# Performance work log

Hardware: AMD Instinct MI355X
Metric: run time of the kernel (lower is better)

## Reference

```python
import jax, jax.numpy as jnp
import numpy as np

NUM_HEADS = 8
HEAD_DIM = 16
HIDDEN = 128  # NUM_HEADS * HEAD_DIM
EPS = 1e-12
NEG_BIG = -1000000.0


def setup_inputs() -> dict:
    key = jax.random.key(0)
    ks = jax.random.split(key, 12)
    bz, n, na, hid = 16, 1024, 32, HIDDEN
    std = 0.02
    return {
        "h": jax.random.normal(ks[0], (bz, n, hid), dtype=jnp.float32),
        "message": jax.random.normal(ks[1], (bz, n, na, hid), dtype=jnp.float32),
        "mask": jax.random.randint(ks[2], (bz, n, na, 1), 0, 2).astype(jnp.float32),
        "qW": jax.random.normal(ks[3], (hid, hid), dtype=jnp.float32) * std,
        "qb": jnp.zeros((hid,), jnp.float32),
        "kW": jax.random.normal(ks[4], (hid, hid), dtype=jnp.float32) * std,
        "kb": jnp.zeros((hid,), jnp.float32),
        "vW": jax.random.normal(ks[5], (hid, hid), dtype=jnp.float32) * std,
        "vb": jnp.zeros((hid,), jnp.float32),
        "dW": jax.random.normal(ks[6], (hid, hid), dtype=jnp.float32) * std,
        "db": jnp.zeros((hid,), jnp.float32),
        "ln_w": jnp.ones((hid,), jnp.float32),
        "ln_b": jnp.zeros((hid,), jnp.float32),
    }


def _layernorm(x, w, b):
    u = jnp.mean(x, axis=-1, keepdims=True)
    s = jnp.mean((x - u) ** 2, axis=-1, keepdims=True)
    return w * ((x - u) / jnp.sqrt(s + EPS)) + b


def reference(h, message, mask, qW, qb, kW, kb, vW, vb, dW, db, ln_w, ln_b):
    bz, n, na, hid = message.shape
    # projections (torch Linear math: x @ W^T + b; here weights stored as [in,out])
    q = h @ qW + qb                              # [b,n,hid]
    k = message @ kW + kb                        # [b,n,na,hid]
    v = jax.nn.relu(message @ vW + vb)           # [b,n,na,hid]
    # split heads
    qh = q.reshape(bz, n, NUM_HEADS, HEAD_DIM)                 # [b,n,h,d] (q_len=1)
    kh = k.reshape(bz, n, na, NUM_HEADS, HEAD_DIM)             # [b,n,k,h,d]
    vh = v.reshape(bz, n, na, NUM_HEADS, HEAD_DIM)
    m = mask[..., 0][:, :, None, :]                            # [b,n,1,k] broadcast over heads
    scores = jnp.einsum("bnhd,bnkhd->bnhk", qh, kh)
    scores = scores / jnp.sqrt(jnp.asarray(HEAD_DIM, scores.dtype)) * m
    scores = jnp.where(scores == 0.0, NEG_BIG, scores)
    probs = jax.nn.softmax(scores, axis=-1) * m                # [b,n,h,k]
    ctx = jnp.einsum("bnhk,bnkhd->bnhd", probs, vh).reshape(bz, n, hid)
    hidden_states = ctx @ dW + db
    return _layernorm(hidden_states + h, ln_w, ln_b)
```

## Files before the change

kernel.cpp:

```cpp
#include <hip/hip_runtime.h>

typedef short  short4v  __attribute__((ext_vector_type(4)));
typedef float  float4v  __attribute__((ext_vector_type(4)));

#define NA   32
#define HID  128
#define NH   8
#define TPB  8
#define KSTR 132

__device__ __forceinline__ unsigned short f2bf(float f) {
  unsigned int u = __float_as_uint(f);
  return (unsigned short)((u + 0x7FFFu + ((u >> 16) & 1u)) >> 16);
}

__global__ __launch_bounds__(256, 2) void soft_attn_mfma(
    const float* __restrict__ h, const float* __restrict__ msg,
    const float* __restrict__ mask,
    const float* __restrict__ qW, const float* __restrict__ qb,
    const float* __restrict__ kW, const float* __restrict__ kb,
    const float* __restrict__ vW, const float* __restrict__ vb,
    const float* __restrict__ dW, const float* __restrict__ db,
    const float* __restrict__ lnw, const float* __restrict__ lnb,
    float* __restrict__ out, int n_tokens)
{
  const int t    = threadIdx.x;
  const int lane = t & 63;
  const int w    = t >> 6;
  const int n0   = w * 32;
  const int lm   = lane & 15;
  const int lg   = lane >> 4;
  const int tok0 = blockIdx.x * TPB;
  if (tok0 >= n_tokens) return;

  __shared__ __align__(16) short s_msgF[16 * 64 * 4];
  __shared__ __align__(16) short s_hF  [ 8 * 64 * 4];
  __shared__ __align__(16) short s_ctxF[ 8 * 64 * 4];
  __shared__ __align__(16) float s_qall[TPB * HID];
  __shared__ __align__(16) float s_hall[TPB * HID];
  __shared__ __align__(16) float s_dall[TPB * HID];
  __shared__ __align__(16) float s_k[NA * KSTR];
  __shared__ __align__(16) float s_v[NA * KSTR];
  __shared__ __align__(16) float s_p[NH * NA];

  {
    ((float4v*)s_hall)[t] = ((const float4v*)(h + (size_t)tok0 * HID))[t];
#pragma unroll
    for (int j = 0; j < 2; ++j) {
      const int s  = t + 256 * j;
      const int f  = s >> 6;
      const int sl = s & 63;
      const int m  = sl & 15, kg = sl >> 4;
      short4v sv = {0, 0, 0, 0};
      if (m < TPB) {
        const float4v hv = *(const float4v*)(h + (size_t)(tok0 + m) * HID + f * 16 + kg * 4);
#pragma unroll
        for (int e = 0; e < 4; ++e) sv[e] = (short)f2bf(hv[e]);
      } else {
        ((short4v*)s_ctxF)[s] = sv;
      }
      ((short4v*)s_hF)[s] = sv;
    }
  }

  {
    short4v Bq[2][8];
    float qb2[2];
#pragma unroll
    for (int nt = 0; nt < 2; ++nt) {
      qb2[nt] = qb[n0 + nt * 16 + lm];
#pragma unroll
      for (int ks = 0; ks < 8; ++ks) {
        short4v bv;
#pragma unroll
        for (int e = 0; e < 4; ++e)
          bv[e] = (short)f2bf(qW[(size_t)(ks * 16 + lg * 4 + e) * HID + n0 + nt * 16 + lm]);
        Bq[nt][ks] = bv;
      }
    }
    __syncthreads();
    float4v accq[2];
#pragma unroll
    for (int nt = 0; nt < 2; ++nt) accq[nt] = (float4v){qb2[nt], qb2[nt], qb2[nt], qb2[nt]};
#pragma unroll
    for (int ks = 0; ks < 8; ++ks) {
      const short4v aq = ((const short4v*)s_hF)[ks * 64 + lane];
#pragma unroll
      for (int nt = 0; nt < 2; ++nt)
        accq[nt] = __builtin_amdgcn_mfma_f32_16x16x16bf16_1k(aq, Bq[nt][ks], accq[nt], 0, 0, 0);
    }
#pragma unroll
    for (int nt = 0; nt < 2; ++nt)
#pragma unroll
      for (int r = 0; r < 4; ++r) {
        const int row = lg * 4 + r;
        if (row < TPB) s_qall[row * HID + n0 + nt * 16 + lm] = accq[nt][r];
      }
  }

  short4v Bk[2][8], Bv[2][8];
  float kb2[2], vb2[2];
#pragma unroll
  for (int nt = 0; nt < 2; ++nt) {
    kb2[nt] = kb[n0 + nt * 16 + lm];
    vb2[nt] = vb[n0 + nt * 16 + lm];
#pragma unroll
    for (int ks = 0; ks < 8; ++ks) {
      short4v bk, bv;
#pragma unroll
      for (int e = 0; e < 4; ++e) {
        const size_t widx = (size_t)(ks * 16 + lg * 4 + e) * HID + n0 + nt * 16 + lm;
        bk[e] = (short)f2bf(kW[widx]);
        bv[e] = (short)f2bf(vW[widx]);
      }
      Bk[nt][ks] = bk; Bv[nt][ks] = bv;
    }
  }

  float4v P[4];
#pragma unroll
  for (int j = 0; j < 4; ++j) {
    const int f = w + 4 * j, mt = f >> 3, ks = f & 7;
    P[j] = *(const float4v*)(msg + (size_t)tok0 * (NA * HID) + (mt * 16 + lm) * HID + ks * 16 + lg * 4);
  }

  for (int it = 0; it < TPB; ++it) {
    const int tok = tok0 + it;

#pragma unroll
    for (int j = 0; j < 4; ++j) {
      const int f = w + 4 * j;
      short4v sv;
#pragma unroll
      for (int e = 0; e < 4; ++e) sv[e] = (short)f2bf(P[j][e]);
      ((short4v*)s_msgF)[f * 64 + lane] = sv;
    }
    __syncthreads();

    if (it + 1 < TPB) {
#pragma unroll
      for (int j = 0; j < 4; ++j) {
        const int f = w + 4 * j, mt = f >> 3, ks = f & 7;
        P[j] = *(const float4v*)(msg + (size_t)(tok + 1) * (NA * HID) + (mt * 16 + lm) * HID + ks * 16 + lg * 4);
      }
    }

#pragma unroll
    for (int mt = 0; mt < 2; ++mt) {
      float4v ak[2], av[2];
#pragma unroll
      for (int nt = 0; nt < 2; ++nt) {
        ak[nt] = (float4v){kb2[nt], kb2[nt], kb2[nt], kb2[nt]};
        av[nt] = (float4v){vb2[nt], vb2[nt], vb2[nt], vb2[nt]};
      }
      short4v af[8];
#pragma unroll
      for (int ks = 0; ks < 8; ++ks)
        af[ks] = ((const short4v*)s_msgF)[(mt * 8 + ks) * 64 + lane];
#pragma unroll
      for (int ks = 0; ks < 8; ++ks)
#pragma unroll
        for (int nt = 0; nt < 2; ++nt) {
          ak[nt] = __builtin_amdgcn_mfma_f32_16x16x16bf16_1k(af[ks], Bk[nt][ks], ak[nt], 0, 0, 0);
          av[nt] = __builtin_amdgcn_mfma_f32_16x16x16bf16_1k(af[ks], Bv[nt][ks], av[nt], 0, 0, 0);
        }
#pragma unroll
      for (int nt = 0; nt < 2; ++nt) {
        const int col  = n0 + nt * 16 + lm;
        const int row0 = mt * 16 + lg * 4;
#pragma unroll
        for (int r = 0; r < 4; ++r) {
          s_k[(row0 + r) * KSTR + col] = ak[nt][r];
          s_v[(row0 + r) * KSTR + col] = fmaxf(av[nt][r], 0.f);
        }
      }
    }
    __syncthreads();

    {
      const int head = t >> 5, a = t & 31;
      const float4v* qr = (const float4v*)(s_qall + it * HID + head * 16);
      const float4v* kr = (const float4v*)(s_k + a * KSTR + head * 16);
      float sc = 0.f;
#pragma unroll
      for (int dd = 0; dd < 4; ++dd) {
        const float4v q4 = qr[dd], k4 = kr[dd];
#pragma unroll
        for (int e = 0; e < 4; ++e) sc = fmaf(q4[e], k4[e], sc);
      }
      const float m = mask[(size_t)tok * NA + a];
      sc = sc * 0.25f * m;
      if (sc == 0.0f) sc = -1000000.0f;
      float mx = sc;
#pragma unroll
      for (int off = 16; off; off >>= 1) mx = fmaxf(mx, __shfl_xor(mx, off));
      const float e = __expf(sc - mx);
      float sm = e;
#pragma unroll
      for (int off = 16; off; off >>= 1) sm += __shfl_xor(sm, off);
      s_p[head * NA + a] = e / sm * m;
    }
    __syncthreads();

    if (t < HID) {
      const int o = t, head = o >> 4;
      float acc = 0.f;
#pragma unroll
      for (int a = 0; a < NA; ++a)
        acc = fmaf(s_p[head * NA + a], s_v[a * KSTR + o], acc);
      ((unsigned short*)s_ctxF)[(o >> 4) * 256 + ((o & 15) >> 2) * 64 + it * 4 + (o & 3)] = f2bf(acc);
    }
  }
  __syncthreads();

  {
    short4v Bd[2][8];
    float db2[2];
#pragma unroll
    for (int nt = 0; nt < 2; ++nt) {
      db2[nt] = db[n0 + nt * 16 + lm];
#pragma unroll
      for (int ks = 0; ks < 8; ++ks) {
        short4v bv;
#pragma unroll
        for (int e = 0; e < 4; ++e)
          bv[e] = (short)f2bf(dW[(size_t)(ks * 16 + lg * 4 + e) * HID + n0 + nt * 16 + lm]);
        Bd[nt][ks] = bv;
      }
    }
    float4v accd[2];
#pragma unroll
    for (int nt = 0; nt < 2; ++nt) accd[nt] = (float4v){db2[nt], db2[nt], db2[nt], db2[nt]};
#pragma unroll
    for (int ks = 0; ks < 8; ++ks) {
      const short4v ad = ((const short4v*)s_ctxF)[ks * 64 + lane];
#pragma unroll
      for (int nt = 0; nt < 2; ++nt)
        accd[nt] = __builtin_amdgcn_mfma_f32_16x16x16bf16_1k(ad, Bd[nt][ks], accd[nt], 0, 0, 0);
    }
#pragma unroll
    for (int nt = 0; nt < 2; ++nt)
#pragma unroll
      for (int r = 0; r < 4; ++r) {
        const int row = lg * 4 + r;
        if (row < TPB) s_dall[row * HID + n0 + nt * 16 + lm] = accd[nt][r];
      }
  }
  __syncthreads();

  {
    const int row = t >> 5, seg = t & 31;
    const float4v xd = *(const float4v*)(s_dall + row * HID + seg * 4);
    const float4v xh = *(const float4v*)(s_hall + row * HID + seg * 4);
    float x[4];
    float s1 = 0.f, s2 = 0.f;
#pragma unroll
    for (int e = 0; e < 4; ++e) { x[e] = xd[e] + xh[e]; s1 += x[e]; s2 += x[e] * x[e]; }
#pragma unroll
    for (int off = 16; off; off >>= 1) { s1 += __shfl_xor(s1, off); s2 += __shfl_xor(s2, off); }
    const float u   = s1 * (1.f / 128.f);
    const float var = s2 * (1.f / 128.f) - u * u;
    const float rs  = rsqrtf(var + 1e-12f);
    const float4v w4 = *(const float4v*)(lnw + seg * 4);
    const float4v b4 = *(const float4v*)(lnb + seg * 4);
    float4v y;
#pragma unroll
    for (int e = 0; e < 4; ++e) y[e] = w4[e] * ((x[e] - u) * rs) + b4[e];
    *(float4v*)(out + (size_t)(tok0 + row) * HID + seg * 4) = y;
  }
}

extern "C" void kernel_launch(void* const* d_in, const int* in_sizes, int n_in,
                              void* d_out, int out_size, void* d_ws, size_t ws_size,
                              hipStream_t stream) {
  const float* h    = (const float*)d_in[0];
  const float* msg  = (const float*)d_in[1];
  const float* mask = (const float*)d_in[2];
  const float* qW   = (const float*)d_in[3];
  const float* qb   = (const float*)d_in[4];
  const float* kW   = (const float*)d_in[5];
  const float* kb   = (const float*)d_in[6];
  const float* vW   = (const float*)d_in[7];
  const float* vb   = (const float*)d_in[8];
  const float* dW   = (const float*)d_in[9];
  const float* db   = (const float*)d_in[10];
  const float* lnw  = (const float*)d_in[11];
  const float* lnb  = (const float*)d_in[12];
  float* out = (float*)d_out;

  const int n_tokens = in_sizes[0] / HID;
  const int nblocks  = n_tokens / TPB;
  soft_attn_mfma<<<nblocks, 256, 0, stream>>>(
      h, msg, mask, qW, qb, kW, kb, vW, vb, dW, db, lnw, lnb, out, n_tokens);
}
```

Baseline: 124.2 us.

## Software-pipeline K/V projection with attention using double-buffered LDS and 16x16x32 MFMA

Restructures the per-token loop so the K/V projection of token i overlaps with the score/softmax/context stage of token i-1. It double-buffers the message fragments and K/V tiles in LDS and cuts the loop from three barriers to one per iteration. It also switches to the 16x16x32 bf16 MFMA with 8-wide fragments, stores K/V in LDS as bf16, and computes the context inside each wave using shuffles instead of a separate probability buffer. This adds a two-deep register prefetch of messages and more register and LDS pressure, which may hurt occupancy at two blocks per CU.

Result: slower. 178.9 us (+44.0%).

```diff
diff --git a/kernel.cpp b/kernel.cpp
--- a/kernel.cpp
+++ b/kernel.cpp
@@ -1,20 +1,23 @@
 #include <hip/hip_runtime.h>
 
-typedef short  short4v  __attribute__((ext_vector_type(4)));
-typedef float  float4v  __attribute__((ext_vector_type(4)));
+typedef short  bf16x8 __attribute__((ext_vector_type(8)));
+typedef float  f32x4  __attribute__((ext_vector_type(4)));
 
 #define NA   32
 #define HID  128
-#define NH   8
 #define TPB  8
-#define KSTR 132
+#define KSTR 136
 
 __device__ __forceinline__ unsigned short f2bf(float f) {
   unsigned int u = __float_as_uint(f);
   return (unsigned short)((u + 0x7FFFu + ((u >> 16) & 1u)) >> 16);
 }
-
-__global__ __launch_bounds__(256, 2) void soft_attn_mfma(
+__device__ __forceinline__ float bf2f(unsigned short s) {
+  return __uint_as_float(((unsigned int)s) << 16);
+}
+
+
+__global__ __launch_bounds__(256, 2) void soft_attn_pipe(
     const float* __restrict__ h, const float* __restrict__ msg,
     const float* __restrict__ mask,
     const float* __restrict__ qW, const float* __restrict__ qb,
@@ -22,72 +25,90 @@
     const float* __restrict__ vW, const float* __restrict__ vb,
     const float* __restrict__ dW, const float* __restrict__ db,
     const float* __restrict__ lnw, const float* __restrict__ lnb,
-    float* __restrict__ out, int n_tokens)
+    float* __restrict__ out)
 {
   const int t    = threadIdx.x;
   const int lane = t & 63;
   const int w    = t >> 6;
-  const int n0   = w * 32;
   const int lm   = lane & 15;
   const int lg   = lane >> 4;
+  const int n0   = w * 32;
   const int tok0 = blockIdx.x * TPB;
-  if (tok0 >= n_tokens) return;
-
-  __shared__ __align__(16) short s_msgF[16 * 64 * 4];
-  __shared__ __align__(16) short s_hF  [ 8 * 64 * 4];
-  __shared__ __align__(16) short s_ctxF[ 8 * 64 * 4];
-  __shared__ __align__(16) float s_qall[TPB * HID];
-  __shared__ __align__(16) float s_hall[TPB * HID];
-  __shared__ __align__(16) float s_dall[TPB * HID];
-  __shared__ __align__(16) float s_k[NA * KSTR];
-  __shared__ __align__(16) float s_v[NA * KSTR];
-  __shared__ __align__(16) float s_p[NH * NA];
-
+
+  __shared__ __align__(16) short          s_msgF[2][8 * 64 * 8];
+  __shared__ __align__(16) unsigned short s_kT[2][NA * KSTR];
+  __shared__ __align__(16) unsigned short s_vT[2][NA * KSTR];
+  __shared__ __align__(16) short          s_hF[4 * 64 * 8];
+  __shared__ __align__(16) short          s_ctxF[4 * 64 * 8];
+  __shared__ __align__(16) float          s_qall[TPB * HID];
+  __shared__ __align__(16) float          s_hall[TPB * HID];
+  __shared__ __align__(16) float          s_dall[TPB * HID];
+
+  ((f32x4*)s_hall)[t] = ((const f32x4*)(h + (size_t)tok0 * HID))[t];
   {
-    ((float4v*)s_hall)[t] = ((const float4v*)(h + (size_t)tok0 * HID))[t];
-#pragma unroll
-    for (int j = 0; j < 2; ++j) {
-      const int s  = t + 256 * j;
-      const int f  = s >> 6;
-      const int sl = s & 63;
-      const int m  = sl & 15, kg = sl >> 4;
-      short4v sv = {0, 0, 0, 0};
-      if (m < TPB) {
-        const float4v hv = *(const float4v*)(h + (size_t)(tok0 + m) * HID + f * 16 + kg * 4);
-#pragma unroll
-        for (int e = 0; e < 4; ++e) sv[e] = (short)f2bf(hv[e]);
-      } else {
-        ((short4v*)s_ctxF)[s] = sv;
-      }
-      ((short4v*)s_hF)[s] = sv;
-    }
-  }
+    const int f = t >> 6, sl = t & 63, m = sl & 15, kg = sl >> 4;
+    bf16x8 sv;
+#pragma unroll
+    for (int e = 0; e < 8; ++e) sv[e] = 0;
+    if (m < TPB) {
+      const float* hp = h + (size_t)(tok0 + m) * HID + f * 32 + kg * 8;
+      const f32x4 x0 = *(const f32x4*)hp;
+      const f32x4 x1 = *(const f32x4*)(hp + 4);
+#pragma unroll
+      for (int e = 0; e < 4; ++e) { sv[e] = (short)f2bf(x0[e]); sv[4 + e] = (short)f2bf(x1[e]); }
+    }
+    ((bf16x8*)s_hF)[t] = sv;
+  }
+#pragma unroll
+  for (int j = 0; j < 2; ++j) {
+    const int s = t + j * 256, f = s >> 6, sl = s & 63, m = sl & 15, kg = sl >> 4;
+    const int mt = f >> 2, ks = f & 3;
+    const float* mp = msg + (size_t)tok0 * (NA * HID) + (mt * 16 + m) * HID + ks * 32 + kg * 8;
+    const f32x4 x0 = *(const f32x4*)mp;
+    const f32x4 x1 = *(const f32x4*)(mp + 4);
+    bf16x8 sv;
+#pragma unroll
+    for (int e = 0; e < 4; ++e) { sv[e] = (short)f2bf(x0[e]); sv[4 + e] = (short)f2bf(x1[e]); }
+    ((bf16x8*)(&s_msgF[0][0]))[s] = sv;
+  }
+
+  bf16x8 Bq[2][4], Bk[2][4], Bv[2][4];
+  float qb2[2], kb2[2], vb2[2];
+#pragma unroll
+  for (int nt = 0; nt < 2; ++nt) {
+    const int col = n0 + nt * 16 + lm;
+    qb2[nt] = qb[col]; kb2[nt] = kb[col]; vb2[nt] = vb[col];
+#pragma unroll
+    for (int ks = 0; ks < 4; ++ks) {
+      bf16x8 bq, bk, bv;
+#pragma unroll
+      for (int e = 0; e < 8; ++e) {
+        const size_t r = (size_t)(ks * 32 + lg * 8 + e) * HID + col;
+        bq[e] = (short)f2bf(qW[r]); bk[e] = (short)f2bf(kW[r]); bv[e] = (short)f2bf(vW[r]);
+      }
+      Bq[nt][ks] = bq; Bk[nt][ks] = bk; Bv[nt][ks] = bv;
+    }
+  }
+
+  f32x4 P[2][2][2];
+#pragma unroll
+  for (int j = 0; j < 2; ++j) {
+    const int f = j * 4 + w, mt = f >> 2, ks = f & 3;
+    const float* mp = msg + (size_t)(tok0 + 1) * (NA * HID) + (mt * 16 + lm) * HID + ks * 32 + lg * 8;
+    P[1][j][0] = *(const f32x4*)mp; P[1][j][1] = *(const f32x4*)(mp + 4);
+  }
+  __syncthreads();
 
   {
-    short4v Bq[2][8];
-    float qb2[2];
-#pragma unroll
-    for (int nt = 0; nt < 2; ++nt) {
-      qb2[nt] = qb[n0 + nt * 16 + lm];
-#pragma unroll
-      for (int ks = 0; ks < 8; ++ks) {
-        short4v bv;
-#pragma unroll
-        for (int e = 0; e < 4; ++e)
-          bv[e] = (short)f2bf(qW[(size_t)(ks * 16 + lg * 4 + e) * HID + n0 + nt * 16 + lm]);
-        Bq[nt][ks] = bv;
-      }
-    }
-    __syncthreads();
-    float4v accq[2];
-#pragma unroll
-    for (int nt = 0; nt < 2; ++nt) accq[nt] = (float4v){qb2[nt], qb2[nt], qb2[nt], qb2[nt]};
-#pragma unroll
-    for (int ks = 0; ks < 8; ++ks) {
-      const short4v aq = ((const short4v*)s_hF)[ks * 64 + lane];
+    f32x4 accq[2];
+#pragma unroll
+    for (int nt = 0; nt < 2; ++nt) accq[nt] = (f32x4){qb2[nt], qb2[nt], qb2[nt], qb2[nt]};
+#pragma unroll
+    for (int ks = 0; ks < 4; ++ks) {
+      const bf16x8 a = ((const bf16x8*)s_hF)[ks * 64 + lane];
 #pragma unroll
       for (int nt = 0; nt < 2; ++nt)
-        accq[nt] = __builtin_amdgcn_mfma_f32_16x16x16bf16_1k(aq, Bq[nt][ks], accq[nt], 0, 0, 0);
+        accq[nt] = __builtin_amdgcn_mfma_f32_16x16x32_bf16(a, Bq[nt][ks], accq[nt], 0, 0, 0);
     }
 #pragma unroll
     for (int nt = 0; nt < 2; ++nt)
@@ -98,145 +119,137 @@
       }
   }
 
-  short4v Bk[2][8], Bv[2][8];
-  float kb2[2], vb2[2];
-#pragma unroll
-  for (int nt = 0; nt < 2; ++nt) {
-    kb2[nt] = kb[n0 + nt * 16 + lm];
-    vb2[nt] = vb[n0 + nt * 16 + lm];
-#pragma unroll
-    for (int ks = 0; ks < 8; ++ks) {
-      short4v bk, bv;
+#pragma unroll
+  for (int it = 0; it <= TPB; ++it) {
+    const int cur = it & 1, nxt = cur ^ 1;
+
+    if (it + 2 < TPB) {
+#pragma unroll
+      for (int j = 0; j < 2; ++j) {
+        const int f = j * 4 + w, mt = f >> 2, ks = f & 3;
+        const float* mp = msg + (size_t)(tok0 + it + 2) * (NA * HID) + (mt * 16 + lm) * HID + ks * 32 + lg * 8;
+        P[cur][j][0] = *(const f32x4*)mp; P[cur][j][1] = *(const f32x4*)(mp + 4);
+      }
+    }
+    if (it + 1 < TPB) {
+#pragma unroll
+      for (int j = 0; j < 2; ++j) {
+        const int f = j * 4 + w;
+        bf16x8 sv;
+#pragma unroll
+        for (int e = 0; e < 4; ++e) {
+          sv[e]     = (short)f2bf(P[nxt][j][0][e]);
+          sv[4 + e] = (short)f2bf(P[nxt][j][1][e]);
+        }
+        ((bf16x8*)(&s_msgF[nxt][0]))[f * 64 + lane] = sv;
+      }
+    }
+    if (it < TPB) {
+      bf16x8 A[2][4];
+#pragma unroll
+      for (int mt = 0; mt < 2; ++mt)
+#pragma unroll
+        for (int ks = 0; ks < 4; ++ks)
+          A[mt][ks] = ((const bf16x8*)(&s_msgF[cur][0]))[(mt * 4 + ks) * 64 + lane];
+      f32x4 ak[2][2], av[2][2];
+#pragma unroll
+      for (int mt = 0; mt < 2; ++mt)
+#pragma unroll
+        for (int nt = 0; nt < 2; ++nt) {
+          ak[mt][nt] = (f32x4){kb2[nt], kb2[nt], kb2[nt], kb2[nt]};
+          av[mt][nt] = (f32x4){vb2[nt], vb2[nt], vb2[nt], vb2[nt]};
+        }
+#pragma unroll
+      for (int ks = 0; ks < 4; ++ks)
+#pragma unroll
+        for (int mt = 0; mt < 2; ++mt)
+#pragma unroll
+          for (int nt = 0; nt < 2; ++nt) {
+            ak[mt][nt] = __builtin_amdgcn_mfma_f32_16x16x32_bf16(A[mt][ks], Bk[nt][ks], ak[mt][nt], 0, 0, 0);
+            av[mt][nt] = __builtin_amdgcn_mfma_f32_16x16x32_bf16(A[mt][ks], Bv[nt][ks], av[mt][nt], 0, 0, 0);
+          }
+#pragma unroll
+      for (int mt = 0; mt < 2; ++mt)
+#pragma unroll
+        for (int nt = 0; nt < 2; ++nt) {
+          const int col = n0 + nt * 16 + lm;
+#pragma unroll
+          for (int r = 0; r < 4; ++r) {
+            const int row = mt * 16 + lg * 4 + r;
+            s_kT[cur][row * KSTR + col] = f2bf(ak[mt][nt][r]);
+            s_vT[cur][row * KSTR + col] = f2bf(fmaxf(av[mt][nt][r], 0.f));
+          }
+        }
+    }
+    if (it > 0) {
+      const int tokA = tok0 + it - 1;
+      const int hh = lane >> 5, a = lane & 31;
+      const int colh = n0 + hh * 16;
+      const f32x4* qr = (const f32x4*)(s_qall + (it - 1) * HID + colh);
+      const bf16x8 k0 = *(const bf16x8*)&s_kT[nxt][a * KSTR + colh];
+      const bf16x8 k1 = *(const bf16x8*)&s_kT[nxt][a * KSTR + colh + 8];
+      const f32x4 q0 = qr[0], q1 = qr[1], q2 = qr[2], q3 = qr[3];
+      float sc = 0.f;
 #pragma unroll
       for (int e = 0; e < 4; ++e) {
-        const size_t widx = (size_t)(ks * 16 + lg * 4 + e) * HID + n0 + nt * 16 + lm;
-        bk[e] = (short)f2bf(kW[widx]);
-        bv[e] = (short)f2bf(vW[widx]);
-      }
-      Bk[nt][ks] = bk; Bv[nt][ks] = bv;
-    }
-  }
-
-  float4v P[4];
-#pragma unroll
-  for (int j = 0; j < 4; ++j) {
-    const int f = w + 4 * j, mt = f >> 3, ks = f & 7;
-    P[j] = *(const float4v*)(msg + (size_t)tok0 * (NA * HID) + (mt * 16 + lm) * HID + ks * 16 + lg * 4);
-  }
-
-  for (int it = 0; it < TPB; ++it) {
-    const int tok = tok0 + it;
-
-#pragma unroll
-    for (int j = 0; j < 4; ++j) {
-      const int f = w + 4 * j;
-      short4v sv;
-#pragma unroll
-      for (int e = 0; e < 4; ++e) sv[e] = (short)f2bf(P[j][e]);
-      ((short4v*)s_msgF)[f * 64 + lane] = sv;
-    }
-    __syncthreads();
-
-    if (it + 1 < TPB) {
-#pragma unroll
-      for (int j = 0; j < 4; ++j) {
-        const int f = w + 4 * j, mt = f >> 3, ks = f & 7;
-        P[j] = *(const float4v*)(msg + (size_t)(tok + 1) * (NA * HID) + (mt * 16 + lm) * HID + ks * 16 + lg * 4);
-      }
-    }
-
-#pragma unroll
-    for (int mt = 0; mt < 2; ++mt) {
-      float4v ak[2], av[2];
-#pragma unroll
-      for (int nt = 0; nt < 2; ++nt) {
-        ak[nt] = (float4v){kb2[nt], kb2[nt], kb2[nt], kb2[nt]};
-        av[nt] = (float4v){vb2[nt], vb2[nt], vb2[nt], vb2[nt]};
-      }
-      short4v af[8];
-#pragma unroll
-      for (int ks = 0; ks < 8; ++ks)
-        af[ks] = ((const short4v*)s_msgF)[(mt * 8 + ks) * 64 + lane];
-#pragma unroll
-      for (int ks = 0; ks < 8; ++ks)
-#pragma unroll
-        for (int nt = 0; nt < 2; ++nt) {
-          ak[nt] = __builtin_amdgcn_mfma_f32_16x16x16bf16_1k(af[ks], Bk[nt][ks], ak[nt], 0, 0, 0);
-          av[nt] = __builtin_amdgcn_mfma_f32_16x16x16bf16_1k(af[ks], Bv[nt][ks], av[nt], 0, 0, 0);
-        }
-#pragma unroll
-      for (int nt = 0; nt < 2; ++nt) {
-        const int col  = n0 + nt * 16 + lm;
-        const int row0 = mt * 16 + lg * 4;
-#pragma unroll
-        for (int r = 0; r < 4; ++r) {
-          s_k[(row0 + r) * KSTR + col] = ak[nt][r];
-          s_v[(row0 + r) * KSTR + col] = fmaxf(av[nt][r], 0.f);
-        }
-      }
-    }
-    __syncthreads();
-
-    {
-      const int head = t >> 5, a = t & 31;
-      const float4v* qr = (const float4v*)(s_qall + it * HID + head * 16);
-      const float4v* kr = (const float4v*)(s_k + a * KSTR + head * 16);
-      float sc = 0.f;
-#pragma unroll
-      for (int dd = 0; dd < 4; ++dd) {
-        const float4v q4 = qr[dd], k4 = kr[dd];
-#pragma unroll
-        for (int e = 0; e < 4; ++e) sc = fmaf(q4[e], k4[e], sc);
-      }
-      const float m = mask[(size_t)tok * NA + a];
-      sc = sc * 0.25f * m;
+        sc = fmaf(q0[e], bf2f((unsigned short)k0[e]), sc);
+        sc = fmaf(q1[e], bf2f((unsigned short)k0[4 + e]), sc);
+        sc = fmaf(q2[e], bf2f((unsigned short)k1[e]), sc);
+        sc = fmaf(q3[e], bf2f((unsigned short)k1[4 + e]), sc);
+      }
+      const float mk = mask[(size_t)tokA * NA + a];
+      sc = sc * 0.25f * mk;
       if (sc == 0.0f) sc = -1000000.0f;
       float mx = sc;
 #pragma unroll
       for (int off = 16; off; off >>= 1) mx = fmaxf(mx, __shfl_xor(mx, off));
-      const float e = __expf(sc - mx);
-      float sm = e;
+      const float ex = __expf(sc - mx);
+      float sm = ex;
 #pragma unroll
       for (int off = 16; off; off >>= 1) sm += __shfl_xor(sm, off);
-      s_p[head * NA + a] = e / sm * m;
+      const float p = ex / sm * mk;
+      const int half = (lane >> 4) & 1;
+      const int colv = colh + lm;
+      float ctx = 0.f;
+#pragma unroll
+      for (int i = 0; i < 16; ++i) {
+        const float pa = __shfl(p, (lane & 32) + half * 16 + i);
+        ctx = fmaf(pa, bf2f(s_vT[nxt][(half * 16 + i) * KSTR + colv]), ctx);
+      }
+      ctx += __shfl_xor(ctx, 16);
+      if (half == 0) {
+        const int col = colv, tk = it - 1;
+        ((unsigned short*)s_ctxF)[((col >> 5) * 64 + tk + ((col & 31) >> 3) * 16) * 8 + (col & 7)] = f2bf(ctx);
+      }
     }
     __syncthreads();
-
-    if (t < HID) {
-      const int o = t, head = o >> 4;
-      float acc = 0.f;
-#pragma unroll
-      for (int a = 0; a < NA; ++a)
-        acc = fmaf(s_p[head * NA + a], s_v[a * KSTR + o], acc);
-      ((unsigned short*)s_ctxF)[(o >> 4) * 256 + ((o & 15) >> 2) * 64 + it * 4 + (o & 3)] = f2bf(acc);
-    }
-  }
-  __syncthreads();
+  }
 
   {
-    short4v Bd[2][8];
+    bf16x8 Bd[2][4];
     float db2[2];
 #pragma unroll
     for (int nt = 0; nt < 2; ++nt) {
-      db2[nt] = db[n0 + nt * 16 + lm];
-#pragma unroll
-      for (int ks = 0; ks < 8; ++ks) {
-        short4v bv;
-#pragma unroll
-        for (int e = 0; e < 4; ++e)
-          bv[e] = (short)f2bf(dW[(size_t)(ks * 16 + lg * 4 + e) * HID + n0 + nt * 16 + lm]);
-        Bd[nt][ks] = bv;
-      }
-    }
-    float4v accd[2];
-#pragma unroll
-    for (int nt = 0; nt < 2; ++nt) accd[nt] = (float4v){db2[nt], db2[nt], db2[nt], db2[nt]};
-#pragma unroll
-    for (int ks = 0; ks < 8; ++ks) {
-      const short4v ad = ((const short4v*)s_ctxF)[ks * 64 + lane];
+      const int col = n0 + nt * 16 + lm;
+      db2[nt] = db[col];
+#pragma unroll
+      for (int ks = 0; ks < 4; ++ks) {
+        bf16x8 bd;
+#pragma unroll
+        for (int e = 0; e < 8; ++e)
+          bd[e] = (short)f2bf(dW[(size_t)(ks * 32 + lg * 8 + e) * HID + col]);
+        Bd[nt][ks] = bd;
+      }
+    }
+    f32x4 accd[2];
+#pragma unroll
+    for (int nt = 0; nt < 2; ++nt) accd[nt] = (f32x4){db2[nt], db2[nt], db2[nt], db2[nt]};
+#pragma unroll
+    for (int ks = 0; ks < 4; ++ks) {
+      const bf16x8 a = ((const bf16x8*)s_ctxF)[ks * 64 + lane];
 #pragma unroll
       for (int nt = 0; nt < 2; ++nt)
-        accd[nt] = __builtin_amdgcn_mfma_f32_16x16x16bf16_1k(ad, Bd[nt][ks], accd[nt], 0, 0, 0);
+        accd[nt] = __builtin_amdgcn_mfma_f32_16x16x32_bf16(a, Bd[nt][ks], accd[nt], 0, 0, 0);
     }
 #pragma unroll
     for (int nt = 0; nt < 2; ++nt)
@@ -250,8 +263,8 @@
 
   {
     const int row = t >> 5, seg = t & 31;
-    const float4v xd = *(const float4v*)(s_dall + row * HID + seg * 4);
-    const float4v xh = *(const float4v*)(s_hall + row * HID + seg * 4);
+    const f32x4 xd = *(const f32x4*)(s_dall + row * HID + seg * 4);
+    const f32x4 xh = *(const f32x4*)(s_hall + row * HID + seg * 4);
     float x[4];
     float s1 = 0.f, s2 = 0.f;
 #pragma unroll
@@ -261,12 +274,12 @@
     const float u   = s1 * (1.f / 128.f);
     const float var = s2 * (1.f / 128.f) - u * u;
     const float rs  = rsqrtf(var + 1e-12f);
-    const float4v w4 = *(const float4v*)(lnw + seg * 4);
-    const float4v b4 = *(const float4v*)(lnb + seg * 4);
-    float4v y;
+    const f32x4 w4 = *(const f32x4*)(lnw + seg * 4);
+    const f32x4 b4 = *(const f32x4*)(lnb + seg * 4);
+    f32x4 y;
 #pragma unroll
     for (int e = 0; e < 4; ++e) y[e] = w4[e] * ((x[e] - u) * rs) + b4[e];
-    *(float4v*)(out + (size_t)(tok0 + row) * HID + seg * 4) = y;
+    *(f32x4*)(out + (size_t)(tok0 + row) * HID + seg * 4) = y;
   }
 }
 
@@ -290,6 +303,6 @@
 
   const int n_tokens = in_sizes[0] / HID;
   const int nblocks  = n_tokens / TPB;
-  soft_attn_mfma<<<nblocks, 256, 0, stream>>>(
-      h, msg, mask, qW, qb, kW, kb, vW, vb, dW, db, lnw, lnb, out, n_tokens);
+  soft_attn_pipe<<<nblocks, 256, 0, stream>>>(
+      h, msg, mask, qW, qb, kW, kb, vW, vb, dW, db, lnw, lnb, out);
 }
```
